# Kernel optimization log

Measured on AMD Instinct MI355X. Metric: run time of the kernel, lower is better.

## Reference

```python
import math
import jax, jax.numpy as jnp
import numpy as np

VOCAB = 50257
MAX_SEQ = 64
D_MODEL = 1024
N_HEADS = 16
N_LAYERS = 12
BATCH = 256
SEQ = 64


def setup_inputs() -> dict:
    key = jax.random.key(0)
    ks = jax.random.split(key, 16)
    s = 0.02
    d, L = D_MODEL, N_LAYERS
    inp = {
        "idx": jax.random.randint(ks[0], (BATCH, SEQ), 0, VOCAB, dtype=jnp.int32),
        "tok_emb": jax.random.normal(ks[1], (VOCAB, d), jnp.float32) * s,
        "pos_emb": jax.random.normal(ks[2], (MAX_SEQ, d), jnp.float32) * s,
        # per-block params stacked over layer dim [L, ...]; linear as x @ W + b
        "wqkv": jax.random.normal(ks[3], (L, d, 3 * d), jnp.float32) * s,
        "bqkv": jnp.zeros((L, 3 * d), jnp.float32),
        "wo": jax.random.normal(ks[4], (L, d, d), jnp.float32) * s,
        "bo": jnp.zeros((L, d), jnp.float32),
        "w1": jax.random.normal(ks[5], (L, d, 4 * d), jnp.float32) * s,
        "b1": jnp.zeros((L, 4 * d), jnp.float32),
        "w2": jax.random.normal(ks[6], (L, 4 * d, d), jnp.float32) * s,
        "b2": jnp.zeros((L, d), jnp.float32),
        "ln_g": jnp.ones((d,), jnp.float32),
        "ln_b": jnp.zeros((d,), jnp.float32),
        "out_w": jax.random.normal(ks[7], (d, d), jnp.float32) * s,
        "out_b": jnp.zeros((d,), jnp.float32),
    }
    return inp


def _attention(x, wqkv_l, bqkv_l, wo_l, bo_l):
    B, S, d = x.shape
    H = N_HEADS
    dh = d // H
    qkv = x @ wqkv_l + bqkv_l                      # [B,S,3d]
    q, k, v = jnp.split(qkv, 3, axis=-1)
    q = q.reshape(B, S, H, dh).transpose(0, 2, 1, 3)  # [B,H,S,dh]
    k = k.reshape(B, S, H, dh).transpose(0, 2, 1, 3)
    v = v.reshape(B, S, H, dh).transpose(0, 2, 1, 3)
    # NOTE: original scales by sqrt(d_model), not sqrt(head_dim)
    attn = jnp.einsum("bhqd,bhkd->bhqk", q, k) / math.sqrt(d)
    causal = jnp.tril(jnp.ones((S, S), bool))       # query i attends key j<=i
    attn = jnp.where(causal[None, None], attn, -jnp.inf)
    # NOTE: original applies softmax over dim=-2 (the QUERY axis)
    attn = jax.nn.softmax(attn, axis=-2)
    y = jnp.einsum("bhqk,bhkd->bhqd", attn, v)      # [B,H,S,dh]
    y = y.transpose(0, 2, 1, 3).reshape(B, S, d)
    return y @ wo_l + bo_l


def _layer_norm(x, g, b, eps=1e-5):
    mu = jnp.mean(x, axis=-1, keepdims=True)
    var = jnp.var(x, axis=-1, keepdims=True)
    return (x - mu) * jax.lax.rsqrt(var + eps) * g + b


def reference(idx, tok_emb, pos_emb, wqkv, bqkv, wo, bo, w1, b1, w2, b2,
              ln_g, ln_b, out_w, out_b):
    S = idx.shape[1]
    x = tok_emb[idx] + pos_emb[:S]                 # [B,S,d]
    for l in range(N_LAYERS):
        x = _attention(x, wqkv[l], bqkv[l], wo[l], bo[l]) + x
        h = jax.nn.gelu(x @ w1[l] + b1[l], approximate=False)
        x = h @ w2[l] + b2[l] + x
    x = _layer_norm(x, ln_g, ln_b)
    return x @ out_w + out_b
```

## Files before the change

### kernel.cpp

```cpp
#include <hip/hip_runtime.h>
#include <stdint.h>

typedef unsigned short u16;
typedef __bf16 bf16x8 __attribute__((ext_vector_type(8)));
typedef float f32x4 __attribute__((ext_vector_type(4)));

#define MT 16384

__device__ __forceinline__ u16 f2bf(float f) {
  union { float f; unsigned u; } x; x.f = f;
  unsigned r = x.u + 0x7fffu + ((x.u >> 16) & 1u);
  return (u16)(r >> 16);
}

#pragma clang diagnostic push
#pragma clang diagnostic ignored "-Waddress-space-conversion"
typedef __attribute__((address_space(1))) unsigned as1u;
typedef __attribute__((address_space(3))) unsigned as3u;
__device__ __forceinline__ void stage16(const u16* g, const u16* lbase) {
  __builtin_amdgcn_global_load_lds((as1u*)g, (as3u*)lbase, 16, 0, 0);
}
#pragma clang diagnostic pop

__global__ void __launch_bounds__(256)
transpose_cvt(const float* __restrict__ in, u16* __restrict__ out, int K, int N) {
  __shared__ float tile[32][33];
  const int k0 = blockIdx.y * 32, n0 = blockIdx.x * 32;
  const int tx = threadIdx.x, ty = threadIdx.y;
  #pragma unroll
  for (int r = 0; r < 32; r += 8)
    tile[ty + r][tx] = in[(size_t)(k0 + ty + r) * N + n0 + tx];
  __syncthreads();
  #pragma unroll
  for (int r = 0; r < 32; r += 8)
    out[(size_t)(n0 + ty + r) * K + k0 + tx] = f2bf(tile[tx][ty + r]);
}

__global__ void __launch_bounds__(256)
embed_kernel(const int* __restrict__ idx, const float* __restrict__ tok,
             const float* __restrict__ pos, float* __restrict__ x,
             u16* __restrict__ xb) {
  const int tk = blockIdx.x;
  const int s = tk & 63;
  const int id = idx[tk];
  const int t = threadIdx.x;
  float4 a = ((const float4*)(tok + (size_t)id * 1024))[t];
  float4 p = ((const float4*)(pos + (size_t)s * 1024))[t];
  float4 r; r.x = a.x + p.x; r.y = a.y + p.y; r.z = a.z + p.z; r.w = a.w + p.w;
  ((float4*)(x + (size_t)tk * 1024))[t] = r;
  u16* o = xb + (size_t)tk * 1024 + t * 4;
  o[0] = f2bf(r.x); o[1] = f2bf(r.y); o[2] = f2bf(r.z); o[3] = f2bf(r.w);
}

template<int EPI>
__global__ void __launch_bounds__(512, 1)
gemm256p(const u16* __restrict__ A, const u16* __restrict__ Bt,
         const float* __restrict__ bias, float* __restrict__ resf,
         u16* __restrict__ outb, float* __restrict__ outf,
         int M, int N, int K, int gn) {
  __shared__ __align__(16) u16 lds[65536];
  const int t = threadIdx.x;
  const int lane = t & 63, w = t >> 6;
  const int wr = w >> 2, wc = w & 3;
  const int fr = lane & 15, fg = lane >> 4;

  const int nwg = gridDim.x;
  const int bid = blockIdx.x;
  const int sw = (bid & 7) * (nwg >> 3) + (bid >> 3);
  const int tn = sw % gn, tm = sw / gn;
  const int m0 = tm * 256, n0 = tn * 256;

  const int srow = w * 32 + (lane >> 2);
  const int scol = (lane & 3) * 8;
  const u16* gA0 = A  + (size_t)(m0 + srow) * K + scol;
  const u16* gA1 = A  + (size_t)(m0 + srow + 16) * K + scol;
  const u16* gB0 = Bt + (size_t)(n0 + srow) * K + scol;
  const u16* gB1 = Bt + (size_t)(n0 + srow + 16) * K + scol;
  const int dA = w * 1024;
  const int dB = 16384 + w * 1024;

  f32x4 acc[8][4] = {};
  const int NT = K >> 6;

  auto STAGE_A = [&](int b, int kh, int ko) {
    stage16(gA0 + ko + kh * 32, &lds[b * 32768 + kh * 8192 + dA]);
    stage16(gA1 + ko + kh * 32, &lds[b * 32768 + kh * 8192 + dA + 512]);
  };
  auto STAGE_B = [&](int b, int kh, int ko) {
    stage16(gB0 + ko + kh * 32, &lds[b * 32768 + kh * 8192 + dB]);
    stage16(gB1 + ko + kh * 32, &lds[b * 32768 + kh * 8192 + dB + 512]);
  };
  auto LDA4 = [&](bf16x8* af, int mq, int kh, int c) {
    #pragma unroll
    for (int m = 0; m < 4; ++m)
      af[m] = *(const bf16x8*)&lds[c * 32768 + kh * 8192 +
                                   (wr * 128 + (mq * 4 + m) * 16 + fr) * 32 + fg * 8];
  };
  auto LDB4 = [&](bf16x8* bv, int kh, int c) {
    #pragma unroll
    for (int n = 0; n < 4; ++n)
      bv[n] = *(const bf16x8*)&lds[c * 32768 + 16384 + kh * 8192 +
                                   (wc * 64 + n * 16 + fr) * 32 + fg * 8];
  };
  auto MFMA16 = [&](bf16x8* af, bf16x8* bv, int mq) {
    __builtin_amdgcn_s_setprio(1);
    #pragma unroll
    for (int m = 0; m < 4; ++m)
      #pragma unroll
      for (int n = 0; n < 4; ++n)
        acc[mq * 4 + m][n] =
            __builtin_amdgcn_mfma_f32_16x16x32_bf16(af[m], bv[n], acc[mq * 4 + m][n], 0, 0, 0);
    __builtin_amdgcn_s_setprio(0);
  };
  #define BARRIER() __builtin_amdgcn_s_barrier()
  #define LGKM0()  asm volatile("s_waitcnt lgkmcnt(0)" ::: "memory")
  #define VMCNT4() asm volatile("s_waitcnt vmcnt(4)" ::: "memory")

  STAGE_A(0, 0, 0); STAGE_B(0, 0, 0);
  STAGE_A(0, 1, 0); STAGE_B(0, 1, 0);
  VMCNT4();
  BARRIER();

  int cur = 0;
  for (int u = 0; u < NT; ++u) {
    const int ko = (u + 1 < NT) ? (u + 1) << 6 : 0;
    const int nb = cur ^ 1;
    bf16x8 bv[4];
    {
      bf16x8 af[4];
      LDA4(af, 0, 0, cur); LDB4(bv, 0, cur);
      STAGE_A(nb, 0, ko);
      BARRIER(); LGKM0();
      MFMA16(af, bv, 0);
      BARRIER();
    }
    {
      bf16x8 af[4];
      LDA4(af, 1, 0, cur);
      STAGE_B(nb, 0, ko);
      VMCNT4();
      BARRIER(); LGKM0();
      MFMA16(af, bv, 1);
      BARRIER();
    }
    {
      bf16x8 af[4];
      LDA4(af, 0, 1, cur); LDB4(bv, 1, cur);
      STAGE_A(nb, 1, ko);
      BARRIER(); LGKM0();
      MFMA16(af, bv, 0);
      BARRIER();
    }
    {
      bf16x8 af[4];
      LDA4(af, 1, 1, cur);
      STAGE_B(nb, 1, ko);
      VMCNT4();
      BARRIER(); LGKM0();
      MFMA16(af, bv, 1);
      BARRIER();
    }
    cur = nb;
  }
  #undef BARRIER
  #undef LGKM0
  #undef VMCNT4

  #pragma unroll
  for (int m = 0; m < 8; ++m) {
    const int row = m0 + wr * 128 + m * 16 + fg * 4;
    #pragma unroll
    for (int n = 0; n < 4; ++n) {
      const int col = n0 + wc * 64 + n * 16 + fr;
      const float bc = bias[col];
      #pragma unroll
      for (int i = 0; i < 4; ++i) {
        const size_t off = (size_t)(row + i) * N + col;
        float v = acc[m][n][i] + bc;
        if constexpr (EPI == 0) {
          outb[off] = f2bf(v);
        } else if constexpr (EPI == 1) {
          v = 0.5f * v * (1.0f + erff(v * 0.70710678118654752f));
          outb[off] = f2bf(v);
        } else if constexpr (EPI == 2) {
          v += resf[off];
          resf[off] = v;
          outb[off] = f2bf(v);
        } else {
          outf[off] = v;
        }
      }
    }
  }
}

__global__ void __launch_bounds__(256)
attn_kernel(const u16* __restrict__ qkv, u16* __restrict__ y) {
  __shared__ __align__(16) u16 qs[64][72];
  __shared__ __align__(16) u16 ks[64][72];
  __shared__ __align__(16) u16 vts[64][72];
  __shared__ __align__(16) float S[64][68];
  __shared__ float red[4][64];

  const int h = blockIdx.x, b = blockIdx.y;
  const int t = threadIdx.x;
  const int lane = t & 63, w = t >> 6;
  const int fr = lane & 15, fg = lane >> 4;

  #pragma unroll
  for (int it = 0; it < 2; ++it) {
    const int id = t + it * 256;
    const int row = id >> 3, seg = id & 7;
    const size_t gq = (size_t)(b * 64 + row) * 3072 + h * 64 + seg * 8;
    *(uint4*)&qs[row][seg * 8] = *(const uint4*)&qkv[gq];
    *(uint4*)&ks[row][seg * 8] = *(const uint4*)&qkv[gq + 1024];
  }
  {
    const int d = t & 63;
    #pragma unroll
    for (int it = 0; it < 16; ++it) {
      const int s = (t >> 6) + it * 4;
      vts[d][s] = qkv[(size_t)(b * 64 + s) * 3072 + 2048 + h * 64 + d];
    }
  }
  __syncthreads();

  f32x4 sa[4] = {};
  #pragma unroll
  for (int kk = 0; kk < 64; kk += 32) {
    bf16x8 qa = *(const bf16x8*)&qs[w * 16 + fr][kk + fg * 8];
    #pragma unroll
    for (int n = 0; n < 4; ++n) {
      bf16x8 kb = *(const bf16x8*)&ks[n * 16 + fr][kk + fg * 8];
      sa[n] = __builtin_amdgcn_mfma_f32_16x16x32_bf16(qa, kb, sa[n], 0, 0, 0);
    }
  }
  #pragma unroll
  for (int n = 0; n < 4; ++n)
    #pragma unroll
    for (int i = 0; i < 4; ++i) {
      const int row = w * 16 + fg * 4 + i, col = n * 16 + fr;
      S[row][col] = (row >= col) ? sa[n][i] * 0.03125f : -1e30f;
    }
  __syncthreads();

  const int c = t & 63, q4 = t >> 6;
  float mx = -1e30f;
  float e[16];
  #pragma unroll
  for (int i = 0; i < 16; ++i) mx = fmaxf(mx, S[q4 * 16 + i][c]);
  red[q4][c] = mx;
  __syncthreads();
  mx = fmaxf(fmaxf(red[0][c], red[1][c]), fmaxf(red[2][c], red[3][c]));
  float sum = 0.f;
  #pragma unroll
  for (int i = 0; i < 16; ++i) { e[i] = __expf(S[q4 * 16 + i][c] - mx); sum += e[i]; }
  __syncthreads();
  red[q4][c] = sum;
  __syncthreads();
  sum = red[0][c] + red[1][c] + red[2][c] + red[3][c];
  const float inv = 1.0f / sum;
  u16 (*P)[72] = qs;
  #pragma unroll
  for (int i = 0; i < 16; ++i)
    P[q4 * 16 + i][c] = f2bf(e[i] * inv);
  __syncthreads();

  f32x4 oa[4] = {};
  #pragma unroll
  for (int kk = 0; kk < 64; kk += 32) {
    bf16x8 pa = *(const bf16x8*)&P[w * 16 + fr][kk + fg * 8];
    #pragma unroll
    for (int n = 0; n < 4; ++n) {
      bf16x8 vb = *(const bf16x8*)&vts[n * 16 + fr][kk + fg * 8];
      oa[n] = __builtin_amdgcn_mfma_f32_16x16x32_bf16(pa, vb, oa[n], 0, 0, 0);
    }
  }
  #pragma unroll
  for (int n = 0; n < 4; ++n)
    #pragma unroll
    for (int i = 0; i < 4; ++i) {
      const int row = w * 16 + fg * 4 + i, col = n * 16 + fr;
      y[(size_t)(b * 64 + row) * 1024 + h * 64 + col] = f2bf(oa[n][i]);
    }
}

__global__ void __launch_bounds__(256)
ln_kernel(const float* __restrict__ x, const float* __restrict__ g,
          const float* __restrict__ bb, u16* __restrict__ xn) {
  __shared__ float sred[8];
  const int tok = blockIdx.x;
  const int t = threadIdx.x;
  const float4 v = ((const float4*)(x + (size_t)tok * 1024))[t];
  float s  = v.x + v.y + v.z + v.w;
  float ss = v.x * v.x + v.y * v.y + v.z * v.z + v.w * v.w;
  #pragma unroll
  for (int o = 32; o > 0; o >>= 1) {
    s  += __shfl_xor(s, o);
    ss += __shfl_xor(ss, o);
  }
  const int w = t >> 6;
  if ((t & 63) == 0) { sred[w] = s; sred[4 + w] = ss; }
  __syncthreads();
  s  = sred[0] + sred[1] + sred[2] + sred[3];
  ss = sred[4] + sred[5] + sred[6] + sred[7];
  const float mu = s * (1.0f / 1024.0f);
  const float var = ss * (1.0f / 1024.0f) - mu * mu;
  const float rs = rsqrtf(var + 1e-5f);
  const float4 gg = ((const float4*)g)[t];
  const float4 b4 = ((const float4*)bb)[t];
  u16* o = xn + (size_t)tok * 1024 + t * 4;
  o[0] = f2bf((v.x - mu) * rs * gg.x + b4.x);
  o[1] = f2bf((v.y - mu) * rs * gg.y + b4.y);
  o[2] = f2bf((v.z - mu) * rs * gg.z + b4.z);
  o[3] = f2bf((v.w - mu) * rs * gg.w + b4.w);
}

extern "C" void kernel_launch(void* const* d_in, const int* in_sizes, int n_in,
                              void* d_out, int out_size, void* d_ws, size_t ws_size,
                              hipStream_t stream) {
  const int*   idx     = (const int*)  d_in[0];
  const float* tok_emb = (const float*)d_in[1];
  const float* pos_emb = (const float*)d_in[2];
  const float* wqkv    = (const float*)d_in[3];
  const float* bqkv    = (const float*)d_in[4];
  const float* wo      = (const float*)d_in[5];
  const float* bo      = (const float*)d_in[6];
  const float* w1      = (const float*)d_in[7];
  const float* b1      = (const float*)d_in[8];
  const float* w2      = (const float*)d_in[9];
  const float* b2      = (const float*)d_in[10];
  const float* ln_g    = (const float*)d_in[11];
  const float* ln_b    = (const float*)d_in[12];
  const float* out_w   = (const float*)d_in[13];
  const float* out_b   = (const float*)d_in[14];

  char* p = (char*)d_ws;
  auto take = [&](size_t n) { char* r = p; p += (n + 255) & ~(size_t)255; return r; };
  u16*   wqkv_t = (u16*)  take((size_t)1024 * 3072 * 2);
  u16*   wo_t   = (u16*)  take((size_t)1024 * 1024 * 2);
  u16*   w1_t   = (u16*)  take((size_t)1024 * 4096 * 2);
  u16*   w2_t   = (u16*)  take((size_t)4096 * 1024 * 2);
  u16*   wout_t = (u16*)  take((size_t)1024 * 1024 * 2);
  float* xf     = (float*)take((size_t)MT * 1024 * 4);
  u16*   xb     = (u16*)  take((size_t)MT * 1024 * 2);
  u16*   yb     = (u16*)  take((size_t)MT * 1024 * 2);
  u16*   big    = (u16*)  take((size_t)MT * 4096 * 2);

  const dim3 tb(32, 8);
  embed_kernel<<<MT, 256, 0, stream>>>(idx, tok_emb, pos_emb, xf, xb);

  for (int l = 0; l < 12; ++l) {
    transpose_cvt<<<dim3(3072 / 32, 1024 / 32), tb, 0, stream>>>(
        wqkv + (size_t)l * 1024 * 3072, wqkv_t, 1024, 3072);
    transpose_cvt<<<dim3(1024 / 32, 1024 / 32), tb, 0, stream>>>(
        wo + (size_t)l * 1024 * 1024, wo_t, 1024, 1024);
    transpose_cvt<<<dim3(4096 / 32, 1024 / 32), tb, 0, stream>>>(
        w1 + (size_t)l * 1024 * 4096, w1_t, 1024, 4096);
    transpose_cvt<<<dim3(1024 / 32, 4096 / 32), tb, 0, stream>>>(
        w2 + (size_t)l * 4096 * 1024, w2_t, 4096, 1024);

    gemm256p<0><<<(MT / 256) * (3072 / 256), 512, 0, stream>>>(
        xb, wqkv_t, bqkv + (size_t)l * 3072,
        nullptr, big, nullptr, MT, 3072, 1024, 3072 / 256);
    attn_kernel<<<dim3(16, 256), 256, 0, stream>>>(big, yb);
    gemm256p<2><<<(MT / 256) * (1024 / 256), 512, 0, stream>>>(
        yb, wo_t, bo + (size_t)l * 1024,
        xf, xb, nullptr, MT, 1024, 1024, 1024 / 256);
    gemm256p<1><<<(MT / 256) * (4096 / 256), 512, 0, stream>>>(
        xb, w1_t, b1 + (size_t)l * 4096,
        nullptr, big, nullptr, MT, 4096, 1024, 4096 / 256);
    gemm256p<2><<<(MT / 256) * (1024 / 256), 512, 0, stream>>>(
        big, w2_t, b2 + (size_t)l * 1024,
        xf, xb, nullptr, MT, 1024, 4096, 1024 / 256);
  }

  transpose_cvt<<<dim3(1024 / 32, 1024 / 32), tb, 0, stream>>>(out_w, wout_t, 1024, 1024);
  ln_kernel<<<MT, 256, 0, stream>>>(xf, ln_g, ln_b, yb);
  gemm256p<3><<<(MT / 256) * (1024 / 256), 512, 0, stream>>>(
      yb, wout_t, out_b, nullptr, nullptr, (float*)d_out, MT, 1024, 1024, 1024 / 256);
}
```

Measured before the change: 7.261 ms.

## Use XOR-swizzled 64-wide LDS tiles and reorder async staging in GEMM

The LDS layout changes from two 32-column k-halves to full 64-column rows, with the 16-byte chunk index XOR-swizzled by row. Fragment reads then avoid bank conflicts. Global-to-LDS staging is regrouped into 64-row chunks, issued in a new order with adjusted vmcnt waits so each chunk arrives before its consumers need it. The added swizzle and wait reordering raise the risk of subtle race or ordering errors.

After: 7.061 ms. 1.03x faster.

```diff
diff --git a/kernel.cpp b/kernel.cpp
--- a/kernel.cpp
+++ b/kernel.cpp
@@ -58,7 +58,7 @@
          const float* __restrict__ bias, float* __restrict__ resf,
          u16* __restrict__ outb, float* __restrict__ outf,
          int M, int N, int K, int gn) {
-  __shared__ __align__(16) u16 lds[65536];
+  __shared__ __align__(16) u16 lds[2][2][16384];
   const int t = threadIdx.x;
   const int lane = t & 63, w = t >> 6;
   const int wr = w >> 2, wc = w & 3;
@@ -70,37 +70,36 @@
   const int tn = sw % gn, tm = sw / gn;
   const int m0 = tm * 256, n0 = tn * 256;
 
-  const int srow = w * 32 + (lane >> 2);
-  const int scol = (lane & 3) * 8;
-  const u16* gA0 = A  + (size_t)(m0 + srow) * K + scol;
-  const u16* gA1 = A  + (size_t)(m0 + srow + 16) * K + scol;
-  const u16* gB0 = Bt + (size_t)(n0 + srow) * K + scol;
-  const u16* gB1 = Bt + (size_t)(n0 + srow + 16) * K + scol;
-  const int dA = w * 1024;
-  const int dB = 16384 + w * 1024;
+  const int srow = w * 8 + (lane >> 3);
+  const int sg = (lane & 7) ^ (lane >> 3);
+  const u16* gA[4]; const u16* gB[4];
+  #pragma unroll
+  for (int c = 0; c < 4; ++c) {
+    gA[c] = A  + (size_t)(m0 + c * 64 + srow) * K + sg * 8;
+    gB[c] = Bt + (size_t)(n0 + c * 64 + srow) * K + sg * 8;
+  }
+  const int lofs = w * 512;
 
   f32x4 acc[8][4] = {};
   const int NT = K >> 6;
 
-  auto STAGE_A = [&](int b, int kh, int ko) {
-    stage16(gA0 + ko + kh * 32, &lds[b * 32768 + kh * 8192 + dA]);
-    stage16(gA1 + ko + kh * 32, &lds[b * 32768 + kh * 8192 + dA + 512]);
+  auto SA = [&](int b, int c, int ko) { stage16(gA[c] + ko, &lds[b][0][lofs + c * 4096]); };
+  auto SB = [&](int b, int c, int ko) { stage16(gB[c] + ko, &lds[b][1][lofs + c * 4096]); };
+  auto LDA4 = [&](bf16x8* af, int mq, int h, int c) {
+    #pragma unroll
+    for (int m = 0; m < 4; ++m) {
+      const int row = wr * 128 + mq * 64 + m * 16 + fr;
+      const int g = (fg + h * 4) ^ (fr & 7);
+      af[m] = *(const bf16x8*)&lds[c][0][row * 64 + g * 8];
+    }
   };
-  auto STAGE_B = [&](int b, int kh, int ko) {
-    stage16(gB0 + ko + kh * 32, &lds[b * 32768 + kh * 8192 + dB]);
-    stage16(gB1 + ko + kh * 32, &lds[b * 32768 + kh * 8192 + dB + 512]);
-  };
-  auto LDA4 = [&](bf16x8* af, int mq, int kh, int c) {
-    #pragma unroll
-    for (int m = 0; m < 4; ++m)
-      af[m] = *(const bf16x8*)&lds[c * 32768 + kh * 8192 +
-                                   (wr * 128 + (mq * 4 + m) * 16 + fr) * 32 + fg * 8];
-  };
-  auto LDB4 = [&](bf16x8* bv, int kh, int c) {
-    #pragma unroll
-    for (int n = 0; n < 4; ++n)
-      bv[n] = *(const bf16x8*)&lds[c * 32768 + 16384 + kh * 8192 +
-                                   (wc * 64 + n * 16 + fr) * 32 + fg * 8];
+  auto LDB4 = [&](bf16x8* bv, int h, int c) {
+    #pragma unroll
+    for (int n = 0; n < 4; ++n) {
+      const int row = wc * 64 + n * 16 + fr;
+      const int g = (fg + h * 4) ^ (fr & 7);
+      bv[n] = *(const bf16x8*)&lds[c][1][row * 64 + g * 8];
+    }
   };
   auto MFMA16 = [&](bf16x8* af, bf16x8* bv, int mq) {
     __builtin_amdgcn_s_setprio(1);
@@ -114,57 +113,57 @@
   };
   #define BARRIER() __builtin_amdgcn_s_barrier()
   #define LGKM0()  asm volatile("s_waitcnt lgkmcnt(0)" ::: "memory")
-  #define VMCNT4() asm volatile("s_waitcnt vmcnt(4)" ::: "memory")
-
-  STAGE_A(0, 0, 0); STAGE_B(0, 0, 0);
-  STAGE_A(0, 1, 0); STAGE_B(0, 1, 0);
-  VMCNT4();
+  #define VMCNT2() asm volatile("s_waitcnt vmcnt(2)" ::: "memory")
+  #define VMCNT0() asm volatile("s_waitcnt vmcnt(0)" ::: "memory")
+
+  SA(0, 0, 0); SA(0, 2, 0);
+  SB(0, 0, 0); SB(0, 1, 0); SB(0, 2, 0); SB(0, 3, 0);
+  SA(0, 1, 0); SA(0, 3, 0);
+  VMCNT2();
   BARRIER();
 
   int cur = 0;
   for (int u = 0; u < NT; ++u) {
     const int ko = (u + 1 < NT) ? (u + 1) << 6 : 0;
     const int nb = cur ^ 1;
-    bf16x8 bv[4];
+    bf16x8 af[4], bv[4];
     {
-      bf16x8 af[4];
       LDA4(af, 0, 0, cur); LDB4(bv, 0, cur);
-      STAGE_A(nb, 0, ko);
+      SA(nb, 0, ko); SA(nb, 2, ko);
+      VMCNT2();
       BARRIER(); LGKM0();
       MFMA16(af, bv, 0);
       BARRIER();
     }
     {
-      bf16x8 af[4];
       LDA4(af, 1, 0, cur);
-      STAGE_B(nb, 0, ko);
-      VMCNT4();
+      SB(nb, 0, ko); SB(nb, 1, ko);
       BARRIER(); LGKM0();
       MFMA16(af, bv, 1);
       BARRIER();
     }
     {
-      bf16x8 af[4];
       LDA4(af, 0, 1, cur); LDB4(bv, 1, cur);
-      STAGE_A(nb, 1, ko);
+      SB(nb, 2, ko); SB(nb, 3, ko);
       BARRIER(); LGKM0();
       MFMA16(af, bv, 0);
       BARRIER();
     }
     {
-      bf16x8 af[4];
       LDA4(af, 1, 1, cur);
-      STAGE_B(nb, 1, ko);
-      VMCNT4();
+      SA(nb, 1, ko); SA(nb, 3, ko);
+      VMCNT2();
       BARRIER(); LGKM0();
       MFMA16(af, bv, 1);
       BARRIER();
     }
     cur = nb;
   }
+  VMCNT0();
   #undef BARRIER
   #undef LGKM0
-  #undef VMCNT4
+  #undef VMCNT2
+  #undef VMCNT0
 
   #pragma unroll
   for (int m = 0; m < 8; ++m) {
```
